# Kernel optimization log

Hardware: AMD Instinct MI355X
Metric: run time of the kernel (lower is better)

Reference implementation:

```python
import jax, jax.numpy as jnp
import numpy as np
from jax import lax

N_STATES = 4096
N_OBS = 512
SEQ_LEN = 8192


def setup_inputs() -> dict:
    key = jax.random.key(0)
    k1, k2, k3 = jax.random.split(key, 3)
    observations = jax.random.randint(k1, (SEQ_LEN,), 0, N_OBS, dtype=jnp.int32)
    # row-stochastic transition matrix (single action, as in TorchCHMMSensory)
    T = jax.random.uniform(k2, (N_STATES, N_STATES), dtype=jnp.float32) + 1e-10
    T = T / T.sum(axis=1, keepdims=True)
    Pi_x = jax.random.uniform(k3, (N_STATES,), dtype=jnp.float32) + 1e-10
    Pi_x = Pi_x / Pi_x.sum()
    return {"T": T, "Pi_x": Pi_x, "observations": observations, "n_observations": N_OBS}


def _forward_backward(T, Pi_x, observations, n_observations):
    """Scaled CHMM forward-backward. Clone-structured deterministic emission:
    state s emits observation s // n_clones, so emission is an indicator mask."""
    S = T.shape[0]
    n_clones = S // n_observations
    state_obs = jnp.arange(S, dtype=jnp.int32) // n_clones  # [S]
    mask = (state_obs[None, :] == observations[:, None]).astype(T.dtype)  # [L, S]

    # --- forward pass (scaled alphas) ---
    a0 = Pi_x * mask[0]
    c0 = a0.sum()
    a0 = a0 / c0

    def fwd_step(alpha, m):
        a = (alpha @ T) * m   # message passing + clone-block restriction
        c = a.sum()
        a = a / c
        return a, (a, c)

    _, (al, cs) = lax.scan(fwd_step, a0, mask[1:])
    alphas = jnp.concatenate([a0[None], al])          # [L, S]
    cs = jnp.concatenate([c0[None], cs])              # [L]
    log_lik = jnp.sum(jnp.log(cs))

    # --- backward pass (scaled betas) ---
    def bwd_step(beta, mc):
        m, c = mc
        b = (T @ (m * beta)) / c
        return b, b

    bL = jnp.ones((S,), dtype=T.dtype)
    _, betas_rev = lax.scan(bwd_step, bL, (mask[1:], cs[1:]), reverse=True)
    betas = jnp.concatenate([betas_rev, bL[None]])    # [L, S]

    gamma = alphas * betas
    gamma = gamma / gamma.sum(axis=1, keepdims=True)  # posteriors [L, S]
    return log_lik, gamma


def reference(T, Pi_x, observations, n_observations):
    return _forward_backward(T, Pi_x, observations, n_observations)
```

## Files before the change

### kernel.cpp

```cpp
#include <hip/hip_runtime.h>


#define NSTATES 4096
#define NBLK    8
#define LSEQ    8192
#define NSTEPS  8191
#define CHK     32
#define NCH     256
#define NGRP    16
#define GSZ     16

#define OFF_P   0u
#define OFF_G2  16384u
#define OFF_LLP 17408u
#define FLG_F1  17664u
#define FLG_F2  17920u
#define FLG_F3  17936u
#define MAGIC   0x5A17C0DEu

__device__ __forceinline__ float aload(float* p) {
    return __hip_atomic_load(p, __ATOMIC_RELAXED, __HIP_MEMORY_SCOPE_AGENT);
}
__device__ __forceinline__ void astore(float* p, float v) {
    __hip_atomic_store(p, v, __ATOMIC_RELAXED, __HIP_MEMORY_SCOPE_AGENT);
}
__device__ __forceinline__ unsigned aloadu(unsigned* p) {
    return __hip_atomic_load(p, __ATOMIC_RELAXED, __HIP_MEMORY_SCOPE_AGENT);
}
__device__ __forceinline__ void astoreu(unsigned* p, unsigned v) {
    __hip_atomic_store(p, v, __ATOMIC_RELAXED, __HIP_MEMORY_SCOPE_AGENT);
}
#define VMFENCE()  asm volatile("s_waitcnt vmcnt(0)" ::: "memory")
#define LDSFENCE() asm volatile("s_waitcnt lgkmcnt(0)" ::: "memory")

__device__ __forceinline__ float exp_renorm(float x, float ref) {
    int k = (int)((__float_as_uint(ref) >> 23) & 0xff) - 127;
    return ldexpf(x, -k);
}

__global__ __launch_bounds__(256) void kFB(const float* __restrict__ T,
                                           const float* __restrict__ Pi,
                                           const int* __restrict__ obs,
                                           float* __restrict__ out,
                                           float* __restrict__ ws)
{
    __shared__ float sM[CHK * 64];
    __shared__ float sDuty[GSZ * 64];
    __shared__ float sG2[NGRP * 64];
    __shared__ float sGP[GSZ * 64];
    __shared__ float sA[(CHK + 1) * 8];
    __shared__ float sB[(CHK + 1) * 8];
    __shared__ float sGv[CHK * 8];
    __shared__ int   sObs[CHK + 1];
    unsigned* flg = reinterpret_cast<unsigned*>(ws);
    const int tid = threadIdx.x;
    const int blk = blockIdx.x;

    if (blk >= NCH) {
        const int c = blk - NCH;
        const int r0 = c * CHK;
        if (tid < CHK + 1) {
            int t = r0 - 1 + tid;
            sObs[tid] = (t >= 0) ? obs[t] : 0;
        }
        __syncthreads();
        float4* o4 = reinterpret_cast<float4*>(out);
        const float4 z = make_float4(0.f, 0.f, 0.f, 0.f);
#pragma unroll 2
        for (int q = tid; q < CHK * 1024; q += 256) {
            int rr = q >> 10, pos = q & 1023;
            int r = r0 + rr;
            int k = r * 1024 + pos;
            int m = r * 1024 + sObs[1 + rr] * 2;
            if (pos != 0 && (unsigned)(k - m) > 2u) o4[k] = z;
        }
        {
            const int rr = tid >> 3, role = tid & 7;
            const int r = r0 + rr;
            const int ob = sObs[1 + rr];
            const int obPrev = sObs[rr];
            const int m = r * 1024 + ob * 2;
            const int ks = r * 1024;
            const bool fullStraddle = (r != 0) && (obPrev != 511) && (ob != 0);
            if (role == 0) {
                if (fullStraddle) o4[ks] = z;
                else if (r != 0 && obPrev != 511) out[(size_t)4 * ks] = 0.f;
            } else if (role <= 3) {
                if (!fullStraddle && ob != 0) out[(size_t)4 * ks + role] = 0.f;
            } else if (role <= 6) {
                if (ob <= 510) out[(size_t)4 * m + 9 + (role - 4)] = 0.f;
            }
            if (tid == 255 && c == NCH - 1 && sObs[CHK] != 511)
                out[(size_t)LSEQ * NSTATES] = 0.f;
        }
        return;
    }

    if (tid >= 64) return;
    const int b = blk;
    const int g = b >> 4, rIn = b & 15;
    const int t0 = b * CHK;
    const int n = min(CHK, NSTEPS - t0);
    float ll0 = 0.f;
    const int i = tid >> 3, j = tid & 7;

    for (int u = tid; u < n * 8; u += 64) {
        int dt = u >> 3, ri = u & 7;
        int t = t0 + dt;
        int row = obs[t] * NBLK + ri;
        int col = obs[t + 1] * NBLK;
        const float4* src = reinterpret_cast<const float4*>(T + (size_t)row * NSTATES + col);
        float4 v0 = src[0], v1 = src[1];
        float vv[8] = {v0.x, v0.y, v0.z, v0.w, v1.x, v1.y, v1.z, v1.w};
        float* base = &sM[dt * 64 + ri];
#pragma unroll
        for (int jj = 0; jj < 8; ++jj) base[jj * 8] = vv[jj];
    }
    if (tid < CHK) sObs[tid] = obs[t0 + tid];
    LDSFENCE();

    {
        float p = sM[j * 8 + i];
        float m[8], mn[8];
#pragma unroll
        for (int k = 0; k < 8; ++k) m[k] = sM[64 + j * 8 + k];
        for (int dt = 1; dt < n; ++dt) {
            int dtn = min(dt + 1, n - 1);
#pragma unroll
            for (int k = 0; k < 8; ++k) mn[k] = sM[dtn * 64 + j * 8 + k];
            float pn = 0.f;
#pragma unroll
            for (int k = 0; k < 8; ++k) pn = fmaf(__shfl(p, i * 8 + k, 64), m[k], pn);
            if ((dt & 3) == 0) pn = exp_renorm(pn, __shfl(pn, 0, 64));
            p = pn;
#pragma unroll
            for (int k = 0; k < 8; ++k) m[k] = mn[k];
        }
        p = exp_renorm(p, __shfl(p, 0, 64));
        astore(&ws[OFF_P + b * 64 + j * 8 + i], p);
    }
    VMFENCE();
    if (tid == 0) astoreu(&flg[FLG_F1 + b], MAGIC);

    if (b < NGRP) {
        for (;;) {
            bool ok = true;
            if (tid < GSZ)
                ok = aloadu(&flg[FLG_F1 + GSZ * b + tid]) == MAGIC;
            if (__all(ok)) break;
            __builtin_amdgcn_s_sleep(1);
        }
        {
            float rb[16];
#pragma unroll
            for (int k = 0; k < 16; ++k)
                rb[k] = aload(&ws[OFF_P + (size_t)b * GSZ * 64 + k * 64 + tid]);
#pragma unroll
            for (int k = 0; k < 16; ++k) sDuty[k * 64 + tid] = rb[k];
        }
        LDSFENCE();
        float p = sDuty[j * 8 + i];
        float m[8], mn[8];
#pragma unroll
        for (int k = 0; k < 8; ++k) m[k] = sDuty[64 + j * 8 + k];
        for (int r = 1; r < GSZ; ++r) {
            int rn = min(r + 1, GSZ - 1);
#pragma unroll
            for (int k = 0; k < 8; ++k) mn[k] = sDuty[rn * 64 + j * 8 + k];
            float pn = 0.f;
#pragma unroll
            for (int k = 0; k < 8; ++k) pn = fmaf(__shfl(p, i * 8 + k, 64), m[k], pn);
            if ((r & 1) == 0 || r == GSZ - 1) pn = exp_renorm(pn, __shfl(pn, 0, 64));
            p = pn;
#pragma unroll
            for (int k = 0; k < 8; ++k) m[k] = mn[k];
        }
        astore(&ws[OFF_G2 + b * 64 + j * 8 + i], p);
        VMFENCE();
        if (tid == 0) astoreu(&flg[FLG_F2 + b], MAGIC);
    }

    for (;;) {
        bool ok = true;
        if (tid < NGRP)
            ok = aloadu(&flg[FLG_F2 + tid]) == MAGIC;
        if (__all(ok)) break;
        __builtin_amdgcn_s_sleep(1);
    }
    {
        float ra[16], rb[16];
#pragma unroll
        for (int k = 0; k < 16; ++k) ra[k] = aload(&ws[OFF_G2 + k * 64 + tid]);
#pragma unroll
        for (int k = 0; k < 16; ++k)
            rb[k] = aload(&ws[OFF_P + (size_t)g * GSZ * 64 + k * 64 + tid]);
#pragma unroll
        for (int k = 0; k < 16; ++k) sG2[k * 64 + tid] = ra[k];
#pragma unroll
        for (int k = 0; k < 16; ++k) sGP[k * 64 + tid] = rb[k];
    }
    LDSFENCE();

    if (tid < 16) {
        const int grp = tid >> 3, l8 = tid & 7;
        const int st = grp ? 8 : 1;
        const int boff = grp ? l8 : l8 * 8;
        float v[8], vb[8];
        {
            float a = Pi[obs[0] * NBLK + l8];
            float s0 = a;
            s0 += __shfl_xor(s0, 1); s0 += __shfl_xor(s0, 2); s0 += __shfl_xor(s0, 4);
            float rs0 = 1.0f / s0;
#pragma unroll
            for (int q = 0; q < 8; ++q) v[q] = grp ? 0.125f : __shfl(a, q, 8) * rs0;
            ll0 = __logf(s0);
        }
        const int cap = grp ? (NGRP - 1 - g) : g;
        if (cap == 0) {
#pragma unroll
            for (int q = 0; q < 8; ++q) vb[q] = v[q];
        }
        for (int r = 0; r < NGRP - 1; ++r) {
            int gi = grp ? (NGRP - 1 - r) : r;
            const float* mb = &sG2[gi * 64 + boff];
            float m[8];
#pragma unroll
            for (int q = 0; q < 8; ++q) m[q] = mb[q * st];
            float u = 0.f;
#pragma unroll
            for (int q = 0; q < 8; ++q) u = fmaf(v[q], m[q], u);
            float s = 0.f;
#pragma unroll
            for (int q = 0; q < 8; ++q) { float x = __shfl(u, q, 8); v[q] = x; s += x; }
            float rs = 1.0f / s;
#pragma unroll
            for (int q = 0; q < 8; ++q) v[q] *= rs;
            if (r + 1 == cap) {
#pragma unroll
                for (int q = 0; q < 8; ++q) vb[q] = v[q];
            }
        }
#pragma unroll
        for (int q = 0; q < 8; ++q) v[q] = vb[q];
        const int cnt = grp ? (GSZ - 1 - rIn) : rIn;
        for (int q = 0; q < GSZ - 1; ++q) {
            bool act = q < cnt;
            int qc = act ? q : 0;
            int lc = grp ? (GSZ - 1 - qc) : qc;
            const float* mb = &sGP[lc * 64 + boff];
            float m[8];
#pragma unroll
            for (int k = 0; k < 8; ++k) m[k] = mb[k * st];
            float u = 0.f;
#pragma unroll
            for (int k = 0; k < 8; ++k) u = fmaf(v[k], m[k], u);
            float s = 0.f;
            float vn[8];
#pragma unroll
            for (int k = 0; k < 8; ++k) { float x = __shfl(u, k, 8); vn[k] = x; s += x; }
            float rs = 1.0f / s;
#pragma unroll
            for (int k = 0; k < 8; ++k) v[k] = act ? vn[k] * rs : v[k];
        }
        float* hist = grp ? sB : sA;
        hist[(grp ? n : 0) * 8 + l8] = v[l8];
        int mt0 = grp ? (n - 1) : 0;
        float m[8], mn[8];
#pragma unroll
        for (int q = 0; q < 8; ++q) m[q] = sM[mt0 * 64 + boff + q * st];
        float ll = 0.f;
        for (int rr = 0; rr < n; ++rr) {
            int rn2 = min(rr + 1, n - 1);
            int mtn = grp ? (n - 1 - rn2) : rn2;
#pragma unroll
            for (int q = 0; q < 8; ++q) mn[q] = sM[mtn * 64 + boff + q * st];
            float u = 0.f;
#pragma unroll
            for (int q = 0; q < 8; ++q) u = fmaf(v[q], m[q], u);
            float s = 0.f;
#pragma unroll
            for (int q = 0; q < 8; ++q) { float x = __shfl(u, q, 8); v[q] = x; s += x; }
            float rs = 1.0f / s;
#pragma unroll
            for (int q = 0; q < 8; ++q) v[q] *= rs;
            hist[(grp ? (n - 1 - rr) : (rr + 1)) * 8 + l8] = v[l8];
            ll += __logf(s);
#pragma unroll
            for (int q = 0; q < 8; ++q) m[q] = mn[q];
        }
        if (tid == 0) astore(&ws[OFF_LLP + b], ll);
    }
    LDSFENCE();

    {
        const int r0l = tid >> 3, ii = tid & 7;
#pragma unroll
        for (int k = 0; k < 4; ++k) {
            int rr = r0l + k * 8;
            float gp = sA[rr * 8 + ii] * sB[rr * 8 + ii];
            float gs = gp;
            gs += __shfl_xor(gs, 1); gs += __shfl_xor(gs, 2); gs += __shfl_xor(gs, 4);
            sGv[rr * 8 + ii] = gp / gs;
        }
    }
    LDSFENCE();
    VMFENCE();
    if (tid == 0) astoreu(&flg[FLG_F3 + b], MAGIC);

    if (tid < CHK) {
        const int r = t0 + tid;
        const int ob = sObs[tid];
        const size_t W = (size_t)r * NSTATES + ob * NBLK;
        const float* gv = &sGv[tid * 8];
        out[W + 1] = gv[0];
        out[W + 2] = gv[1];
        out[W + 3] = gv[2];
        reinterpret_cast<float4*>(out)[W / 4 + 1] = make_float4(gv[3], gv[4], gv[5], gv[6]);
        out[W + 8] = gv[7];
    }

    if (b == 0) {
        for (;;) {
            bool ok = true;
#pragma unroll
            for (int q = 0; q < 4; ++q)
                ok = ok && (aloadu(&flg[FLG_F3 + tid * 4 + q]) == MAGIC);
            if (__all(ok)) break;
            __builtin_amdgcn_s_sleep(1);
        }
        float part = 0.f;
#pragma unroll
        for (int q = 0; q < 4; ++q) part += aload(&ws[OFF_LLP + tid * 4 + q]);
        part += __shfl_xor(part, 32); part += __shfl_xor(part, 16);
        part += __shfl_xor(part, 8);  part += __shfl_xor(part, 4);
        part += __shfl_xor(part, 2);  part += __shfl_xor(part, 1);
        if (tid == 0) out[0] = part + ll0;
    }
}

extern "C" void kernel_launch(void* const* d_in, const int* in_sizes, int n_in,
                              void* d_out, int out_size, void* d_ws, size_t ws_size,
                              hipStream_t stream)
{
    const float* T   = (const float*)d_in[0];
    const float* Pi  = (const float*)d_in[1];
    const int*   obs = (const int*)d_in[2];
    float* out = (float*)d_out;
    float* ws  = (float*)d_ws;

    kFB<<<NCH * 2, 256, 0, stream>>>(T, Pi, obs, out, ws);
}
```

Measured before the change: 41.86 us.

## Split zero-fill into more blocks with nontemporal stores and compute log-likelihood from exponent tracking

The zero-fill work for the large gamma output moves from 256 blocks of 32 rows each to 1024 blocks of 8 rows each, and it now uses nontemporal float4 stores. The straddle handling is simplified to match. The per-chunk log-likelihood is no longer summed as a log per step inside the forward history loop. Instead it comes from the accumulated power-of-two renormalisation exponents plus one final dot product against the group product. The aim is to spread the store-bound fill across more CUs, bypass cache pollution, and take the log out of the serial loop. The risk is a numerical difference in how the log-likelihood is assembled.

```diff
diff --git a/kernel.cpp b/kernel.cpp
--- a/kernel.cpp
+++ b/kernel.cpp
@@ -9,6 +9,8 @@
 #define NCH     256
 #define NGRP    16
 #define GSZ     16
+#define NFILL   1024
+#define FROWS   8
 
 #define OFF_P   0u
 #define OFF_G2  16384u
@@ -33,9 +35,14 @@
 #define VMFENCE()  asm volatile("s_waitcnt vmcnt(0)" ::: "memory")
 #define LDSFENCE() asm volatile("s_waitcnt lgkmcnt(0)" ::: "memory")
 
-__device__ __forceinline__ float exp_renorm(float x, float ref) {
-    int k = (int)((__float_as_uint(ref) >> 23) & 0xff) - 127;
-    return ldexpf(x, -k);
+typedef float floatx4 __attribute__((ext_vector_type(4)));
+__device__ __forceinline__ void ntz4(float4* p) {
+    floatx4 z = {0.f, 0.f, 0.f, 0.f};
+    __builtin_nontemporal_store(z, reinterpret_cast<floatx4*>(p));
+}
+
+__device__ __forceinline__ int expof(float x) {
+    return (int)((__float_as_uint(x) >> 23) & 0xff) - 127;
 }
 
 __global__ __launch_bounds__(256) void kFB(const float* __restrict__ T,
@@ -57,42 +64,39 @@
     const int blk = blockIdx.x;
 
     if (blk >= NCH) {
-        const int c = blk - NCH;
-        const int r0 = c * CHK;
-        if (tid < CHK + 1) {
+        const int f = blk - NCH;
+        const int r0 = f * FROWS;
+        if (tid < FROWS + 1) {
             int t = r0 - 1 + tid;
             sObs[tid] = (t >= 0) ? obs[t] : 0;
         }
         __syncthreads();
         float4* o4 = reinterpret_cast<float4*>(out);
-        const float4 z = make_float4(0.f, 0.f, 0.f, 0.f);
-#pragma unroll 2
-        for (int q = tid; q < CHK * 1024; q += 256) {
+#pragma unroll 4
+        for (int q = tid; q < FROWS * 1024; q += 256) {
             int rr = q >> 10, pos = q & 1023;
-            int r = r0 + rr;
-            int k = r * 1024 + pos;
-            int m = r * 1024 + sObs[1 + rr] * 2;
-            if (pos != 0 && (unsigned)(k - m) > 2u) o4[k] = z;
-        }
-        {
+            int w2 = sObs[1 + rr] * 2;
+            if (pos != 0 && (unsigned)(pos - w2) > 2u)
+                ntz4(&o4[(r0 + rr) * 1024 + pos]);
+        }
+        if (tid < FROWS * 8) {
             const int rr = tid >> 3, role = tid & 7;
             const int r = r0 + rr;
             const int ob = sObs[1 + rr];
             const int obPrev = sObs[rr];
-            const int m = r * 1024 + ob * 2;
-            const int ks = r * 1024;
-            const bool fullStraddle = (r != 0) && (obPrev != 511) && (ob != 0);
+            const size_t rowBase = (size_t)r * 4096;
             if (role == 0) {
-                if (fullStraddle) o4[ks] = z;
-                else if (r != 0 && obPrev != 511) out[(size_t)4 * ks] = 0.f;
+                if (r != 0 && obPrev != 511) out[rowBase] = 0.f;
             } else if (role <= 3) {
-                if (!fullStraddle && ob != 0) out[(size_t)4 * ks + role] = 0.f;
+                if (ob != 0) out[rowBase + role] = 0.f;
             } else if (role <= 6) {
-                if (ob <= 510) out[(size_t)4 * m + 9 + (role - 4)] = 0.f;
+                if (ob <= 510) out[rowBase + 8 * ob + 9 + (role - 4)] = 0.f;
+            } else {
+                if (ob >= 1) out[rowBase + 8 * ob] = 0.f;
             }
-            if (tid == 255 && c == NCH - 1 && sObs[CHK] != 511)
-                out[(size_t)LSEQ * NSTATES] = 0.f;
-        }
+        }
+        if (f == NFILL - 1 && tid == 255 && sObs[FROWS] != 511)
+            out[(size_t)LSEQ * NSTATES] = 0.f;
         return;
     }
 
@@ -102,6 +106,7 @@
     const int t0 = b * CHK;
     const int n = min(CHK, NSTEPS - t0);
     float ll0 = 0.f;
+    int kTot = 0;
     const int i = tid >> 3, j = tid & 7;
 
     for (int u = tid; u < n * 8; u += 64) {
@@ -131,12 +136,20 @@
             float pn = 0.f;
 #pragma unroll
             for (int k = 0; k < 8; ++k) pn = fmaf(__shfl(p, i * 8 + k, 64), m[k], pn);
-            if ((dt & 3) == 0) pn = exp_renorm(pn, __shfl(pn, 0, 64));
+            if ((dt & 3) == 0) {
+                int ke = expof(__shfl(pn, 0, 64));
+                pn = ldexpf(pn, -ke);
+                kTot += ke;
+            }
             p = pn;
 #pragma unroll
             for (int k = 0; k < 8; ++k) m[k] = mn[k];
         }
-        p = exp_renorm(p, __shfl(p, 0, 64));
+        {
+            int ke = expof(__shfl(p, 0, 64));
+            p = ldexpf(p, -ke);
+            kTot += ke;
+        }
         astore(&ws[OFF_P + b * 64 + j * 8 + i], p);
     }
     VMFENCE();
@@ -170,7 +183,10 @@
             float pn = 0.f;
 #pragma unroll
             for (int k = 0; k < 8; ++k) pn = fmaf(__shfl(p, i * 8 + k, 64), m[k], pn);
-            if ((r & 1) == 0 || r == GSZ - 1) pn = exp_renorm(pn, __shfl(pn, 0, 64));
+            if ((r & 1) == 0 || r == GSZ - 1) {
+                int ke = expof(__shfl(pn, 0, 64));
+                pn = ldexpf(pn, -ke);
+            }
             p = pn;
 #pragma unroll
             for (int k = 0; k < 8; ++k) m[k] = mn[k];
@@ -262,13 +278,22 @@
 #pragma unroll
             for (int k = 0; k < 8; ++k) v[k] = act ? vn[k] * rs : v[k];
         }
+        if (grp == 0) {
+            float u = 0.f;
+#pragma unroll
+            for (int q2 = 0; q2 < 8; ++q2)
+                u = fmaf(v[q2], sGP[rIn * 64 + l8 * 8 + q2], u);
+            float ssum = u;
+            ssum += __shfl_xor(ssum, 1); ssum += __shfl_xor(ssum, 2); ssum += __shfl_xor(ssum, 4);
+            if (l8 == 0)
+                astore(&ws[OFF_LLP + b], __logf(ssum) + (float)kTot * 0.69314718055994531f);
+        }
         float* hist = grp ? sB : sA;
         hist[(grp ? n : 0) * 8 + l8] = v[l8];
         int mt0 = grp ? (n - 1) : 0;
         float m[8], mn[8];
 #pragma unroll
         for (int q = 0; q < 8; ++q) m[q] = sM[mt0 * 64 + boff + q * st];
-        float ll = 0.f;
         for (int rr = 0; rr < n; ++rr) {
             int rn2 = min(rr + 1, n - 1);
             int mtn = grp ? (n - 1 - rn2) : rn2;
@@ -284,11 +309,9 @@
 #pragma unroll
             for (int q = 0; q < 8; ++q) v[q] *= rs;
             hist[(grp ? (n - 1 - rr) : (rr + 1)) * 8 + l8] = v[l8];
-            ll += __logf(s);
 #pragma unroll
             for (int q = 0; q < 8; ++q) m[q] = mn[q];
         }
-        if (tid == 0) astore(&ws[OFF_LLP + b], ll);
     }
     LDSFENCE();
 
@@ -348,5 +371,5 @@
     float* out = (float*)d_out;
     float* ws  = (float*)d_ws;
 
-    kFB<<<NCH * 2, 256, 0, stream>>>(T, Pi, obs, out, ws);
-}
+    kFB<<<NCH + NFILL, 256, 0, stream>>>(T, Pi, obs, out, ws);
+}
```

Result: slower. 46.57 us (+11.2%).
